# Kernel optimization log

Hardware: AMD Instinct MI355X
Metric: run time of the kernel (lower is better)

## Reference

```python
import jax, jax.numpy as jnp
import numpy as np

B, S, D = 2, 2048, 4096
H, KVH, HD = 32, 8, 128   # attention heads, kv heads, head_dim
GROUPS = H // KVH          # 4
SCALING = 0.08838834764831845  # attention_multiplier = 1/sqrt(head_dim)
NEG = -1e9


def _rope_tables(seq_len, head_dim, base=10000.0):
    half = head_dim // 2
    inv_freq = 1.0 / (base ** (np.arange(0, half, dtype=np.float32) / half))
    t = np.arange(seq_len, dtype=np.float32)
    freqs = np.outer(t, inv_freq)               # [S, half]
    emb = np.concatenate([freqs, freqs], axis=-1)  # [S, head_dim]
    return jnp.asarray(np.cos(emb)), jnp.asarray(np.sin(emb))


def setup_inputs() -> dict:
    key = jax.random.key(0)
    ks = jax.random.split(key, 6)
    hidden_states = jax.random.normal(ks[0], (B, S, D), dtype=jnp.float32)
    std = 0.02
    Wq = jax.random.normal(ks[1], (D, H * HD), dtype=jnp.float32) * std
    Wk = jax.random.normal(ks[2], (D, KVH * HD), dtype=jnp.float32) * std
    Wv = jax.random.normal(ks[3], (D, KVH * HD), dtype=jnp.float32) * std
    Wo = jax.random.normal(ks[4], (H * HD, D), dtype=jnp.float32) * std
    cos1, sin1 = _rope_tables(S, HD)
    cos = jnp.broadcast_to(cos1[None], (B, S, HD))
    sin = jnp.broadcast_to(sin1[None], (B, S, HD))
    # additive causal mask [B, 1, S, S]
    causal = jnp.where(jnp.tril(jnp.ones((S, S), dtype=bool)), 0.0, NEG).astype(jnp.float32)
    attention_mask = jnp.broadcast_to(causal[None, None], (B, 1, S, S))
    return {"hidden_states": hidden_states, "cos": cos, "sin": sin,
            "attention_mask": attention_mask, "Wq": Wq, "Wk": Wk, "Wv": Wv, "Wo": Wo}


def _rotate_half(x):
    x1, x2 = jnp.split(x, 2, axis=-1)
    return jnp.concatenate([-x2, x1], axis=-1)


def reference(hidden_states, cos, sin, attention_mask, Wq, Wk, Wv, Wo):
    b, s, _ = hidden_states.shape
    # projections (no bias), split into heads: [B, H, S, HD]
    q = jnp.einsum('bsd,de->bse', hidden_states, Wq).reshape(b, s, H, HD).transpose(0, 2, 1, 3)
    k = jnp.einsum('bsd,de->bse', hidden_states, Wk).reshape(b, s, KVH, HD).transpose(0, 2, 1, 3)
    v = jnp.einsum('bsd,de->bse', hidden_states, Wv).reshape(b, s, KVH, HD).transpose(0, 2, 1, 3)
    # RoPE (cos/sin unsqueezed on head dim)
    c = cos[:, None, :, :]
    sn = sin[:, None, :, :]
    q = q * c + _rotate_half(q) * sn
    k = k * c + _rotate_half(k) * sn
    # repeat_kv: [B, KVH, S, HD] -> [B, H, S, HD]
    k = jnp.repeat(k, GROUPS, axis=1)
    v = jnp.repeat(v, GROUPS, axis=1)
    # eager attention: full score matrix, additive mask, fp32 softmax
    scores = jnp.einsum('bhqd,bhkd->bhqk', q, k) * SCALING + attention_mask
    attn_weights = jax.nn.softmax(scores.astype(jnp.float32), axis=-1).astype(q.dtype)
    attn_output = jnp.einsum('bhqk,bhkd->bhqd', attn_weights, v)
    attn_output = attn_output.transpose(0, 2, 1, 3).reshape(b, s, H * HD)
    attn_output = jnp.einsum('bse,ed->bsd', attn_output, Wo)
    return attn_output, attn_weights
```

## Files before the change

### kernel.cpp

```cpp
#include <hip/hip_runtime.h>

typedef unsigned short u16;
typedef unsigned int u32;
typedef __attribute__((ext_vector_type(8))) short bf16x8;
typedef __attribute__((ext_vector_type(4))) float f32x4;

#define SCALING 0.08838834764831845f

__device__ __forceinline__ float bf2f(u16 u) {
  union { u32 i; float f; } v; v.i = ((u32)u) << 16; return v.f;
}
__device__ __forceinline__ u16 f2bf(float f) {
  union { float f; u32 i; } v; v.f = f;
  u32 x = v.i;
  return (u16)((x + 0x7fffu + ((x >> 16) & 1u)) >> 16);
}

__device__ __forceinline__ void gll16(const void* g, void* l) {
  __builtin_amdgcn_global_load_lds((const __attribute__((address_space(1))) void*)g,
                                   (__attribute__((address_space(3))) void*)l, 16, 0, 0);
}

__global__ void cast_f32_to_bf16(const float* __restrict__ in, u16* __restrict__ out, int n4) {
  int i = blockIdx.x * 256 + threadIdx.x;
  if (i >= n4) return;
  float4 v = ((const float4*)in)[i];
  ushort4 o;
  o.x = f2bf(v.x); o.y = f2bf(v.y); o.z = f2bf(v.z); o.w = f2bf(v.w);
  ((ushort4*)out)[i] = o;
}

__global__ void transpose_cast(const float* __restrict__ W, u16* __restrict__ WT, int Kd, int Nd) {
  __shared__ float tile[32][33];
  int n0 = blockIdx.x * 32, k0 = blockIdx.y * 32;
  int t = threadIdx.x;
  int r = t >> 3;
  int c = (t & 7) * 4;
  float4 v = *(const float4*)(W + (size_t)(k0 + r) * Nd + n0 + c);
  tile[r][c + 0] = v.x; tile[r][c + 1] = v.y; tile[r][c + 2] = v.z; tile[r][c + 3] = v.w;
  __syncthreads();
  ushort4 o;
  o.x = f2bf(tile[c + 0][r]); o.y = f2bf(tile[c + 1][r]);
  o.z = f2bf(tile[c + 2][r]); o.w = f2bf(tile[c + 3][r]);
  *(ushort4*)(WT + (size_t)(n0 + r) * Kd + k0 + c) = o;
}

template <bool OUT_F32>
__global__ __launch_bounds__(256) void gemm_bt(const u16* __restrict__ A, const u16* __restrict__ B,
                                               void* __restrict__ C, int M, int N, int K) {
  __shared__ __align__(16) u16 As[128 * 32];
  __shared__ __align__(16) u16 Bs[128 * 32];
  const int tid = threadIdx.x;
  const int lane = tid & 63;
  const int w = tid >> 6;
  const int wr = w >> 1, wc = w & 1;
  const int q = lane >> 4, cl = lane & 15;
  const int m0 = blockIdx.y * 128, n0 = blockIdx.x * 128;

  const int srow = w * 16 + (lane >> 2);
  const int schk = (lane & 3) * 8;
  const u16* Ag0 = A + (size_t)(m0 + srow) * K + schk;
  const u16* Ag1 = Ag0 + (size_t)64 * K;
  const u16* Bg0 = B + (size_t)(n0 + srow) * K + schk;
  const u16* Bg1 = Bg0 + (size_t)64 * K;
  u16* Asp = As + srow * 32 + schk;
  u16* Bsp = Bs + srow * 32 + schk;

  f32x4 zero4 = {0.f, 0.f, 0.f, 0.f};
  f32x4 acc[4][4];
#pragma unroll
  for (int mi = 0; mi < 4; ++mi)
#pragma unroll
    for (int ni = 0; ni < 4; ++ni) acc[mi][ni] = zero4;

  for (int kk = 0; kk < K; kk += 32) {
    gll16(Ag0 + kk, Asp);
    gll16(Ag1 + kk, Asp + 64 * 32);
    gll16(Bg0 + kk, Bsp);
    gll16(Bg1 + kk, Bsp + 64 * 32);
    __syncthreads();
    bf16x8 af[4], bfv[4];
#pragma unroll
    for (int mi = 0; mi < 4; ++mi)
      af[mi] = *(const bf16x8*)(As + (wr * 64 + mi * 16 + cl) * 32 + q * 8);
#pragma unroll
    for (int ni = 0; ni < 4; ++ni)
      bfv[ni] = *(const bf16x8*)(Bs + (wc * 64 + ni * 16 + cl) * 32 + q * 8);
#pragma unroll
    for (int mi = 0; mi < 4; ++mi)
#pragma unroll
      for (int ni = 0; ni < 4; ++ni)
        acc[mi][ni] = __builtin_amdgcn_mfma_f32_16x16x32_bf16(af[mi], bfv[ni], acc[mi][ni], 0, 0, 0);
    __syncthreads();
  }

#pragma unroll
  for (int mi = 0; mi < 4; ++mi)
#pragma unroll
    for (int ni = 0; ni < 4; ++ni) {
      int row = m0 + wr * 64 + mi * 16 + q * 4;
      int col = n0 + wc * 64 + ni * 16 + cl;
#pragma unroll
      for (int r = 0; r < 4; ++r) {
        if (OUT_F32)
          ((float*)C)[(size_t)(row + r) * N + col] = acc[mi][ni][r];
        else
          ((u16*)C)[(size_t)(row + r) * N + col] = f2bf(acc[mi][ni][r]);
      }
    }
}

__global__ void rope_kernel(u16* __restrict__ X, const float* __restrict__ cosb,
                            const float* __restrict__ sinb, int rowstride) {
  int row = blockIdx.x;
  int v = blockIdx.y * 256 + threadIdx.x;
  int d = v & 63, hh = v >> 6;
  size_t base = (size_t)row * rowstride + hh * 128 + d;
  float x1 = bf2f(X[base]);
  float x2 = bf2f(X[base + 64]);
  const float* cp = cosb + (size_t)row * 128;
  const float* sp = sinb + (size_t)row * 128;
  X[base]      = f2bf(x1 * cp[d]      - x2 * sp[d]);
  X[base + 64] = f2bf(x2 * cp[d + 64] + x1 * sp[d + 64]);
}

__global__ __launch_bounds__(512, 4) void attn_kernel(
    const u16* __restrict__ Qb, const u16* __restrict__ Kb, const u16* __restrict__ Vb,
    float* __restrict__ Wout, u16* __restrict__ AO) {
  const int qt = blockIdx.x;
  const int h = blockIdx.y;
  const int b = blockIdx.z;
  const int kvh = h >> 2;

  __shared__ __align__(16) u16 Ksm[2][64 * 128];
  __shared__ __align__(16) u32 Vt[128 * 32];
  __shared__ __align__(16) u16 Ps[128 * 64];
  __shared__ float l_lds[128];

  const int tid = threadIdx.x;
  const int lane = tid & 63;
  const int w = tid >> 6;
  const int wr = w >> 1, wc = w & 1;
  const int q = lane >> 4, cl = lane & 15;
  const int cx = cl & 7;

  const size_t qrow0 = (size_t)b * 2048 + qt * 128;
  const u16* Qh = Qb + qrow0 * 4096 + h * 128;
  const u16* Kh = Kb + ((size_t)b * 2048) * 1024 + kvh * 128;
  const u16* Vh = Vb + ((size_t)b * 2048) * 1024 + kvh * 128;

  bf16x8 qa[2][4];
#pragma unroll
  for (int mi = 0; mi < 2; ++mi) {
    const u16* qp = Qh + (size_t)(wr * 32 + mi * 16 + cl) * 4096 + q * 8;
#pragma unroll
    for (int kd = 0; kd < 4; ++kd) qa[mi][kd] = *(const bf16x8*)(qp + kd * 32);
  }

  if (tid < 128) l_lds[tid] = 0.f;

  const int srow = tid >> 4;
  const int kchunk = (tid & 15) ^ (srow & 7);
  const int njt = 2 * qt + 2;

  auto stageK = [&](int jt, int buf) {
    const u16* s0 = Kh + ((size_t)(jt * 64 + srow)) * 1024 + kchunk * 8;
    u16* d0 = Ksm[buf] + tid * 8;
    gll16(s0, d0);
    gll16(s0 + 32 * 1024, d0 + 4096);
  };

  f32x4 zero4 = {0.f, 0.f, 0.f, 0.f};

  float lpart[2][4];
#pragma unroll
  for (int mi = 0; mi < 2; ++mi)
#pragma unroll
    for (int r = 0; r < 4; ++r) lpart[mi][r] = 0.f;

  stageK(0, 0);
  for (int t = 0; t < njt; ++t) {
    __syncthreads();
    if (t + 1 < njt) stageK(t + 1, (t + 1) & 1);
    const u16* Kc = Ksm[t & 1];
    f32x4 acc[2][2];
#pragma unroll
    for (int mi = 0; mi < 2; ++mi)
#pragma unroll
      for (int ni = 0; ni < 2; ++ni) acc[mi][ni] = zero4;
    __builtin_amdgcn_s_setprio(1);
#pragma unroll
    for (int kd = 0; kd < 4; ++kd) {
      bf16x8 bk[2];
#pragma unroll
      for (int ni = 0; ni < 2; ++ni) {
        int row = wc * 32 + ni * 16 + cl;
        bk[ni] = *(const bf16x8*)(Kc + row * 128 + (((kd * 4 + q) ^ cx) << 3));
      }
#pragma unroll
      for (int mi = 0; mi < 2; ++mi)
#pragma unroll
        for (int ni = 0; ni < 2; ++ni)
          acc[mi][ni] = __builtin_amdgcn_mfma_f32_16x16x32_bf16(qa[mi][kd], bk[ni], acc[mi][ni], 0, 0, 0);
    }
    __builtin_amdgcn_s_setprio(0);
    if (t >= 2 * qt) {
#pragma unroll
      for (int mi = 0; mi < 2; ++mi)
#pragma unroll
        for (int r = 0; r < 4; ++r) {
          int ig = qt * 128 + wr * 32 + mi * 16 + q * 4 + r;
          float s = 0.f;
#pragma unroll
          for (int ni = 0; ni < 2; ++ni) {
            int jg = t * 64 + wc * 32 + ni * 16 + cl;
            s += (jg <= ig) ? __expf(acc[mi][ni][r] * SCALING) : 0.f;
          }
          lpart[mi][r] += s;
        }
    } else {
#pragma unroll
      for (int mi = 0; mi < 2; ++mi)
#pragma unroll
        for (int r = 0; r < 4; ++r) {
          float s = 0.f;
#pragma unroll
          for (int ni = 0; ni < 2; ++ni) s += __expf(acc[mi][ni][r] * SCALING);
          lpart[mi][r] += s;
        }
    }
  }
#pragma unroll
  for (int mi = 0; mi < 2; ++mi)
#pragma unroll
    for (int r = 0; r < 4; ++r) {
      float v = lpart[mi][r];
      v += __shfl_xor(v, 1, 64);
      v += __shfl_xor(v, 2, 64);
      v += __shfl_xor(v, 4, 64);
      v += __shfl_xor(v, 8, 64);
      if (cl == 0) atomicAdd(&l_lds[wr * 32 + mi * 16 + q * 4 + r], v);
    }
  __syncthreads();
  float rv[2][4];
#pragma unroll
  for (int mi = 0; mi < 2; ++mi)
#pragma unroll
    for (int r = 0; r < 4; ++r) rv[mi][r] = 1.f / l_lds[wr * 32 + mi * 16 + q * 4 + r];

  f32x4 oacc[2][4];
#pragma unroll
  for (int mi = 0; mi < 2; ++mi)
#pragma unroll
    for (int nd = 0; nd < 4; ++nd) oacc[mi][nd] = zero4;

  const int vp = tid >> 4;
  const int vc = tid & 15;
  const int vd0 = vc * 8;

  stageK(0, 0);
  for (int t = 0; t < njt; ++t) {
    __syncthreads();

    const u16* vsrc = Vh + ((size_t)(t * 64 + 2 * vp)) * 1024 + vd0;
    uint4 va = *(const uint4*)vsrc;
    uint4 vb4 = *(const uint4*)(vsrc + 1024);

    const u16* Kc = Ksm[t & 1];
    f32x4 acc[2][2];
#pragma unroll
    for (int mi = 0; mi < 2; ++mi)
#pragma unroll
      for (int ni = 0; ni < 2; ++ni) acc[mi][ni] = zero4;
    __builtin_amdgcn_s_setprio(1);
#pragma unroll
    for (int kd = 0; kd < 4; ++kd) {
      bf16x8 bk[2];
#pragma unroll
      for (int ni = 0; ni < 2; ++ni) {
        int row = wc * 32 + ni * 16 + cl;
        bk[ni] = *(const bf16x8*)(Kc + row * 128 + (((kd * 4 + q) ^ cx) << 3));
      }
#pragma unroll
      for (int mi = 0; mi < 2; ++mi)
#pragma unroll
        for (int ni = 0; ni < 2; ++ni)
          acc[mi][ni] = __builtin_amdgcn_mfma_f32_16x16x32_bf16(qa[mi][kd], bk[ni], acc[mi][ni], 0, 0, 0);
    }
    __builtin_amdgcn_s_setprio(0);

    {
      const u16* ah = (const u16*)&va;
      const u16* bh = (const u16*)&vb4;
#pragma unroll
      for (int kk = 0; kk < 8; ++kk) {
        int k = (kk + vc) & 7;
        int d = vd0 + k;
        Vt[d * 32 + ((((vp >> 2) ^ k) << 2) | (vp & 3))] = (u32)ah[k] | ((u32)bh[k] << 16);
      }
    }

    {
      bool diag = (t >= 2 * qt);
#pragma unroll
      for (int mi = 0; mi < 2; ++mi)
#pragma unroll
        for (int r = 0; r < 4; ++r) {
          int row = wr * 32 + mi * 16 + q * 4 + r;
          int ig = qt * 128 + row;
          float rvv = rv[mi][r];
#pragma unroll
          for (int ni = 0; ni < 2; ++ni) {
            int col = wc * 32 + ni * 16 + cl;
            float p = __expf(acc[mi][ni][r] * SCALING) * rvv;
            if (diag) { int jg = t * 64 + col; p = (jg <= ig) ? p : 0.f; }
            Ps[row * 64 + (((col >> 3) ^ (row & 7)) << 3) + (col & 7)] = f2bf(p);
          }
        }
    }

    if (t + 1 < njt) stageK(t + 1, (t + 1) & 1);

    asm volatile("s_waitcnt lgkmcnt(0)\n\ts_barrier" ::: "memory");

    {
      float* wb = Wout + (((size_t)(b * 32 + h) * 2048 + qt * 128) * 2048) + (size_t)t * 64;
#pragma unroll
      for (int it = 0; it < 2; ++it) {
        int cf = tid + it * 512;
        int row = cf >> 3;
        int ch = (cf & 7) * 8;
        bf16x8 pv8 = *(const bf16x8*)(Ps + row * 64 + (((ch >> 3) ^ (row & 7)) << 3));
        float4 o0 = {bf2f((u16)pv8[0]), bf2f((u16)pv8[1]), bf2f((u16)pv8[2]), bf2f((u16)pv8[3])};
        float4 o1 = {bf2f((u16)pv8[4]), bf2f((u16)pv8[5]), bf2f((u16)pv8[6]), bf2f((u16)pv8[7])};
        float* dp = wb + (size_t)row * 2048 + ch;
        *(float4*)dp = o0;
        *(float4*)(dp + 4) = o1;
      }
    }

    {
      __builtin_amdgcn_s_setprio(1);
#pragma unroll
      for (int ks = 0; ks < 2; ++ks) {
        bf16x8 pa[2], vbf[4];
#pragma unroll
        for (int mi = 0; mi < 2; ++mi) {
          int row = wr * 32 + mi * 16 + cl;
          pa[mi] = *(const bf16x8*)(Ps + row * 64 + (((ks * 4 + q) ^ cx) << 3));
        }
#pragma unroll
        for (int nd = 0; nd < 4; ++nd) {
          int d = wc * 64 + nd * 16 + cl;
          vbf[nd] = *(const bf16x8*)((const u16*)Vt + d * 64 + (((ks * 4 + q) ^ cx) << 3));
        }
#pragma unroll
        for (int mi = 0; mi < 2; ++mi)
#pragma unroll
          for (int nd = 0; nd < 4; ++nd)
            oacc[mi][nd] = __builtin_amdgcn_mfma_f32_16x16x32_bf16(pa[mi], vbf[nd], oacc[mi][nd], 0, 0, 0);
      }
      __builtin_amdgcn_s_setprio(0);
    }
  }

  {
    float* wb0 = Wout + (((size_t)(b * 32 + h) * 2048 + qt * 128) * 2048);
    float4 z = {0.f, 0.f, 0.f, 0.f};
    for (int jt = njt; jt < 32; ++jt) {
      float* wbz = wb0 + (size_t)jt * 64;
#pragma unroll
      for (int it = 0; it < 2; ++it) {
        int cf = tid + it * 512;
        int row = cf >> 3;
        int ch = (cf & 7) * 8;
        float* dp = wbz + (size_t)row * 2048 + ch;
        *(float4*)dp = z;
        *(float4*)(dp + 4) = z;
      }
    }
  }

#pragma unroll
  for (int mi = 0; mi < 2; ++mi)
#pragma unroll
    for (int nd = 0; nd < 4; ++nd) {
      int il = wr * 32 + mi * 16 + q * 4;
      int d = wc * 64 + nd * 16 + cl;
#pragma unroll
      for (int r = 0; r < 4; ++r)
        AO[(qrow0 + il + r) * 4096 + h * 128 + d] = f2bf(oacc[mi][nd][r]);
    }
}

extern "C" void kernel_launch(void* const* d_in, const int* in_sizes, int n_in,
                              void* d_out, int out_size, void* d_ws, size_t ws_size,
                              hipStream_t stream) {
  const float* hidden = (const float*)d_in[0];
  const float* cosb = (const float*)d_in[1];
  const float* sinb = (const float*)d_in[2];
  const float* Wq = (const float*)d_in[4];
  const float* Wk = (const float*)d_in[5];
  const float* Wv = (const float*)d_in[6];
  const float* Wo = (const float*)d_in[7];

  char* ws = (char*)d_ws;
  u16* hb  = (u16*)(ws);
  u16* WqT = (u16*)(ws + 33554432L);
  u16* WkT = (u16*)(ws + 67108864L);
  u16* WvT = (u16*)(ws + 75497472L);
  u16* WoT = (u16*)(ws + 83886080L);
  u16* Qb  = (u16*)(ws + 117440512L);
  u16* Kb  = (u16*)(ws + 150994944L);
  u16* Vb  = (u16*)(ws + 159383552L);
  u16* AO  = WqT;

  float* out0 = (float*)d_out;
  float* out1 = out0 + 16777216L;

  cast_f32_to_bf16<<<16384, 256, 0, stream>>>(hidden, hb, 4194304);
  transpose_cast<<<dim3(128, 128), 256, 0, stream>>>(Wq, WqT, 4096, 4096);
  transpose_cast<<<dim3(32, 128), 256, 0, stream>>>(Wk, WkT, 4096, 1024);
  transpose_cast<<<dim3(32, 128), 256, 0, stream>>>(Wv, WvT, 4096, 1024);
  transpose_cast<<<dim3(128, 128), 256, 0, stream>>>(Wo, WoT, 4096, 4096);

  gemm_bt<false><<<dim3(32, 32), 256, 0, stream>>>(hb, WqT, Qb, 4096, 4096, 4096);
  gemm_bt<false><<<dim3(8, 32), 256, 0, stream>>>(hb, WkT, Kb, 4096, 1024, 4096);
  gemm_bt<false><<<dim3(8, 32), 256, 0, stream>>>(hb, WvT, Vb, 4096, 1024, 4096);

  rope_kernel<<<dim3(4096, 8), 256, 0, stream>>>(Qb, cosb, sinb, 4096);
  rope_kernel<<<dim3(4096, 2), 256, 0, stream>>>(Kb, cosb, sinb, 1024);

  attn_kernel<<<dim3(16, 32, 2), 512, 0, stream>>>(Qb, Kb, Vb, out1, AO);

  gemm_bt<true><<<dim3(32, 32), 256, 0, stream>>>(AO, WoT, out0, 4096, 4096, 4096);
}
```

Baseline: 2.805 ms.

## Pair causal query tiles per block, map KV groups to XCDs, prefetch V

Each attention block now processes two query tiles (qp and 15-qp) so every block does the same causal work. A flat 512-block grid is remapped so that blocks sharing a (batch, kv-head) group land on the same XCD, which should improve L2 reuse of K/V. V rows for the next tile are now prefetched into registers during the current tile, with explicit waitcnt barriers. This halves the block count and adds register pressure, and it depends on the waitcnt counts being exactly right.

```diff
diff --git a/kernel.cpp b/kernel.cpp
--- a/kernel.cpp
+++ b/kernel.cpp
@@ -127,10 +127,13 @@
 __global__ __launch_bounds__(512, 4) void attn_kernel(
     const u16* __restrict__ Qb, const u16* __restrict__ Kb, const u16* __restrict__ Vb,
     float* __restrict__ Wout, u16* __restrict__ AO) {
-  const int qt = blockIdx.x;
-  const int h = blockIdx.y;
-  const int b = blockIdx.z;
-  const int kvh = h >> 2;
+  const int flat = blockIdx.x;
+  const int xcd = flat & 7, slot = flat >> 3;
+  const int grp = xcd * 2 + (slot >> 5);
+  const int mem = slot & 31;
+  const int b = grp & 1, kvh = grp >> 1;
+  const int h = kvh * 4 + (mem & 3);
+  const int qp = mem >> 2;
 
   __shared__ __align__(16) u16 Ksm[2][64 * 128];
   __shared__ __align__(16) u32 Vt[128 * 32];
@@ -144,24 +147,14 @@
   const int q = lane >> 4, cl = lane & 15;
   const int cx = cl & 7;
 
-  const size_t qrow0 = (size_t)b * 2048 + qt * 128;
-  const u16* Qh = Qb + qrow0 * 4096 + h * 128;
   const u16* Kh = Kb + ((size_t)b * 2048) * 1024 + kvh * 128;
   const u16* Vh = Vb + ((size_t)b * 2048) * 1024 + kvh * 128;
 
-  bf16x8 qa[2][4];
-#pragma unroll
-  for (int mi = 0; mi < 2; ++mi) {
-    const u16* qp = Qh + (size_t)(wr * 32 + mi * 16 + cl) * 4096 + q * 8;
-#pragma unroll
-    for (int kd = 0; kd < 4; ++kd) qa[mi][kd] = *(const bf16x8*)(qp + kd * 32);
-  }
-
-  if (tid < 128) l_lds[tid] = 0.f;
-
   const int srow = tid >> 4;
   const int kchunk = (tid & 15) ^ (srow & 7);
-  const int njt = 2 * qt + 2;
+  const int vp = tid >> 4;
+  const int vc = tid & 15;
+  const int vd0 = vc * 8;
 
   auto stageK = [&](int jt, int buf) {
     const u16* s0 = Kh + ((size_t)(jt * 64 + srow)) * 1024 + kchunk * 8;
@@ -172,225 +165,252 @@
 
   f32x4 zero4 = {0.f, 0.f, 0.f, 0.f};
 
-  float lpart[2][4];
-#pragma unroll
-  for (int mi = 0; mi < 2; ++mi)
-#pragma unroll
-    for (int r = 0; r < 4; ++r) lpart[mi][r] = 0.f;
-
-  stageK(0, 0);
-  for (int t = 0; t < njt; ++t) {
+  for (int half = 0; half < 2; ++half) {
+    const int qt = half ? (15 - qp) : qp;
+    const int njt = 2 * qt + 2;
+    const size_t qrow0 = (size_t)b * 2048 + qt * 128;
+    const u16* Qh = Qb + qrow0 * 4096 + h * 128;
+
     __syncthreads();
-    if (t + 1 < njt) stageK(t + 1, (t + 1) & 1);
-    const u16* Kc = Ksm[t & 1];
-    f32x4 acc[2][2];
+    if (tid < 128) l_lds[tid] = 0.f;
+
+    bf16x8 qa[2][4];
+#pragma unroll
+    for (int mi = 0; mi < 2; ++mi) {
+      const u16* qp_ = Qh + (size_t)(wr * 32 + mi * 16 + cl) * 4096 + q * 8;
+#pragma unroll
+      for (int kd = 0; kd < 4; ++kd) qa[mi][kd] = *(const bf16x8*)(qp_ + kd * 32);
+    }
+
+    float lpart[2][4];
 #pragma unroll
     for (int mi = 0; mi < 2; ++mi)
 #pragma unroll
-      for (int ni = 0; ni < 2; ++ni) acc[mi][ni] = zero4;
-    __builtin_amdgcn_s_setprio(1);
-#pragma unroll
-    for (int kd = 0; kd < 4; ++kd) {
-      bf16x8 bk[2];
-#pragma unroll
-      for (int ni = 0; ni < 2; ++ni) {
-        int row = wc * 32 + ni * 16 + cl;
-        bk[ni] = *(const bf16x8*)(Kc + row * 128 + (((kd * 4 + q) ^ cx) << 3));
-      }
+      for (int r = 0; r < 4; ++r) lpart[mi][r] = 0.f;
+
+    stageK(0, 0);
+    __syncthreads();
+    for (int t = 0; t < njt; ++t) {
+      if (t + 1 < njt) stageK(t + 1, (t + 1) & 1);
+      const u16* Kc = Ksm[t & 1];
+      f32x4 acc[2][2];
 #pragma unroll
       for (int mi = 0; mi < 2; ++mi)
 #pragma unroll
-        for (int ni = 0; ni < 2; ++ni)
-          acc[mi][ni] = __builtin_amdgcn_mfma_f32_16x16x32_bf16(qa[mi][kd], bk[ni], acc[mi][ni], 0, 0, 0);
-    }
-    __builtin_amdgcn_s_setprio(0);
-    if (t >= 2 * qt) {
+        for (int ni = 0; ni < 2; ++ni) acc[mi][ni] = zero4;
+      __builtin_amdgcn_s_setprio(1);
+#pragma unroll
+      for (int kd = 0; kd < 4; ++kd) {
+        bf16x8 bk[2];
+#pragma unroll
+        for (int ni = 0; ni < 2; ++ni) {
+          int row = wc * 32 + ni * 16 + cl;
+          bk[ni] = *(const bf16x8*)(Kc + row * 128 + (((kd * 4 + q) ^ cx) << 3));
+        }
+#pragma unroll
+        for (int mi = 0; mi < 2; ++mi)
+#pragma unroll
+          for (int ni = 0; ni < 2; ++ni)
+            acc[mi][ni] = __builtin_amdgcn_mfma_f32_16x16x32_bf16(qa[mi][kd], bk[ni], acc[mi][ni], 0, 0, 0);
+      }
+      __builtin_amdgcn_s_setprio(0);
+      if (t >= 2 * qt) {
+#pragma unroll
+        for (int mi = 0; mi < 2; ++mi)
+#pragma unroll
+          for (int r = 0; r < 4; ++r) {
+            int ig = qt * 128 + wr * 32 + mi * 16 + q * 4 + r;
+            float s = 0.f;
+#pragma unroll
+            for (int ni = 0; ni < 2; ++ni) {
+              int jg = t * 64 + wc * 32 + ni * 16 + cl;
+              s += (jg <= ig) ? __expf(acc[mi][ni][r] * SCALING) : 0.f;
+            }
+            lpart[mi][r] += s;
+          }
+      } else {
+#pragma unroll
+        for (int mi = 0; mi < 2; ++mi)
+#pragma unroll
+          for (int r = 0; r < 4; ++r) {
+            float s = 0.f;
+#pragma unroll
+            for (int ni = 0; ni < 2; ++ni) s += __expf(acc[mi][ni][r] * SCALING);
+            lpart[mi][r] += s;
+          }
+      }
+      if (t + 1 < njt) __syncthreads();
+    }
+#pragma unroll
+    for (int mi = 0; mi < 2; ++mi)
+#pragma unroll
+      for (int r = 0; r < 4; ++r) {
+        float v = lpart[mi][r];
+        v += __shfl_xor(v, 1, 64);
+        v += __shfl_xor(v, 2, 64);
+        v += __shfl_xor(v, 4, 64);
+        v += __shfl_xor(v, 8, 64);
+        if (cl == 0) atomicAdd(&l_lds[wr * 32 + mi * 16 + q * 4 + r], v);
+      }
+    __syncthreads();
+    float rv[2][4];
+#pragma unroll
+    for (int mi = 0; mi < 2; ++mi)
+#pragma unroll
+      for (int r = 0; r < 4; ++r) rv[mi][r] = 1.f / l_lds[wr * 32 + mi * 16 + q * 4 + r];
+
+    f32x4 oacc[2][4];
+#pragma unroll
+    for (int mi = 0; mi < 2; ++mi)
+#pragma unroll
+      for (int nd = 0; nd < 4; ++nd) oacc[mi][nd] = zero4;
+
+    uint4 vca, vcb, vna, vnb;
+    stageK(0, 0);
+    {
+      const u16* vsrc = Vh + ((size_t)(2 * vp)) * 1024 + vd0;
+      vca = *(const uint4*)vsrc;
+      vcb = *(const uint4*)(vsrc + 1024);
+    }
+    asm volatile("s_waitcnt vmcnt(2) lgkmcnt(0)\n\ts_barrier" ::: "memory");
+
+    for (int t = 0; t < njt; ++t) {
+      if (t + 1 < njt) {
+        stageK(t + 1, (t + 1) & 1);
+        const u16* vsrc = Vh + ((size_t)((t + 1) * 64 + 2 * vp)) * 1024 + vd0;
+        vna = *(const uint4*)vsrc;
+        vnb = *(const uint4*)(vsrc + 1024);
+      }
+
+      const u16* Kc = Ksm[t & 1];
+      f32x4 acc[2][2];
 #pragma unroll
       for (int mi = 0; mi < 2; ++mi)
 #pragma unroll
-        for (int r = 0; r < 4; ++r) {
-          int ig = qt * 128 + wr * 32 + mi * 16 + q * 4 + r;
-          float s = 0.f;
-#pragma unroll
-          for (int ni = 0; ni < 2; ++ni) {
-            int jg = t * 64 + wc * 32 + ni * 16 + cl;
-            s += (jg <= ig) ? __expf(acc[mi][ni][r] * SCALING) : 0.f;
+        for (int ni = 0; ni < 2; ++ni) acc[mi][ni] = zero4;
+      __builtin_amdgcn_s_setprio(1);
+#pragma unroll
+      for (int kd = 0; kd < 4; ++kd) {
+        bf16x8 bk[2];
+#pragma unroll
+        for (int ni = 0; ni < 2; ++ni) {
+          int row = wc * 32 + ni * 16 + cl;
+          bk[ni] = *(const bf16x8*)(Kc + row * 128 + (((kd * 4 + q) ^ cx) << 3));
+        }
+#pragma unroll
+        for (int mi = 0; mi < 2; ++mi)
+#pragma unroll
+          for (int ni = 0; ni < 2; ++ni)
+            acc[mi][ni] = __builtin_amdgcn_mfma_f32_16x16x32_bf16(qa[mi][kd], bk[ni], acc[mi][ni], 0, 0, 0);
+      }
+      __builtin_amdgcn_s_setprio(0);
+
+      {
+        const u16* ah = (const u16*)&vca;
+        const u16* bh = (const u16*)&vcb;
+#pragma unroll
+        for (int kk = 0; kk < 8; ++kk) {
+          int k = (kk + vc) & 7;
+          int d = vd0 + k;
+          Vt[d * 32 + ((((vp >> 2) ^ k) << 2) | (vp & 3))] = (u32)ah[k] | ((u32)bh[k] << 16);
+        }
+      }
+
+      {
+        bool diag = (t >= 2 * qt);
+#pragma unroll
+        for (int mi = 0; mi < 2; ++mi)
+#pragma unroll
+          for (int r = 0; r < 4; ++r) {
+            int row = wr * 32 + mi * 16 + q * 4 + r;
+            int ig = qt * 128 + row;
+            float rvv = rv[mi][r];
+#pragma unroll
+            for (int ni = 0; ni < 2; ++ni) {
+              int col = wc * 32 + ni * 16 + cl;
+              float p = __expf(acc[mi][ni][r] * SCALING) * rvv;
+              if (diag) { int jg = t * 64 + col; p = (jg <= ig) ? p : 0.f; }
+              Ps[row * 64 + (((col >> 3) ^ (row & 7)) << 3) + (col & 7)] = f2bf(p);
+            }
           }
-          lpart[mi][r] += s;
-        }
-    } else {
-#pragma unroll
-      for (int mi = 0; mi < 2; ++mi)
-#pragma unroll
-        for (int r = 0; r < 4; ++r) {
-          float s = 0.f;
-#pragma unroll
-          for (int ni = 0; ni < 2; ++ni) s += __expf(acc[mi][ni][r] * SCALING);
-          lpart[mi][r] += s;
-        }
-    }
+      }
+
+      asm volatile("s_waitcnt lgkmcnt(0)\n\ts_barrier" ::: "memory");
+
+      {
+        float* wb = Wout + (((size_t)(b * 32 + h) * 2048 + qt * 128) * 2048) + (size_t)t * 64;
+#pragma unroll
+        for (int it = 0; it < 2; ++it) {
+          int cf = tid + it * 512;
+          int row = cf >> 3;
+          int ch = (cf & 7) * 8;
+          bf16x8 pv8 = *(const bf16x8*)(Ps + row * 64 + (((ch >> 3) ^ (row & 7)) << 3));
+          float4 o0 = {bf2f((u16)pv8[0]), bf2f((u16)pv8[1]), bf2f((u16)pv8[2]), bf2f((u16)pv8[3])};
+          float4 o1 = {bf2f((u16)pv8[4]), bf2f((u16)pv8[5]), bf2f((u16)pv8[6]), bf2f((u16)pv8[7])};
+          float* dp = wb + (size_t)row * 2048 + ch;
+          *(float4*)dp = o0;
+          *(float4*)(dp + 4) = o1;
+        }
+      }
+
+      {
+        __builtin_amdgcn_s_setprio(1);
+#pragma unroll
+        for (int ks = 0; ks < 2; ++ks) {
+          bf16x8 pa[2], vbf[4];
+#pragma unroll
+          for (int mi = 0; mi < 2; ++mi) {
+            int row = wr * 32 + mi * 16 + cl;
+            pa[mi] = *(const bf16x8*)(Ps + row * 64 + (((ks * 4 + q) ^ cx) << 3));
+          }
+#pragma unroll
+          for (int nd = 0; nd < 4; ++nd) {
+            int d = wc * 64 + nd * 16 + cl;
+            vbf[nd] = *(const bf16x8*)((const u16*)Vt + d * 64 + (((ks * 4 + q) ^ cx) << 3));
+          }
+#pragma unroll
+          for (int mi = 0; mi < 2; ++mi)
+#pragma unroll
+            for (int nd = 0; nd < 4; ++nd)
+              oacc[mi][nd] = __builtin_amdgcn_mfma_f32_16x16x32_bf16(pa[mi], vbf[nd], oacc[mi][nd], 0, 0, 0);
+        }
+        __builtin_amdgcn_s_setprio(0);
+      }
+
+      if (t + 1 < njt) {
+        vca = vna; vcb = vnb;
+        asm volatile("s_waitcnt vmcnt(6) lgkmcnt(0)\n\ts_barrier" ::: "memory");
+      }
+    }
+
+    {
+      float* wb0 = Wout + (((size_t)(b * 32 + h) * 2048 + qt * 128) * 2048);
+      float4 z = {0.f, 0.f, 0.f, 0.f};
+      for (int jt = njt; jt < 32; ++jt) {
+        float* wbz = wb0 + (size_t)jt * 64;
+#pragma unroll
+        for (int it = 0; it < 2; ++it) {
+          int cf = tid + it * 512;
+          int row = cf >> 3;
+          int ch = (cf & 7) * 8;
+          float* dp = wbz + (size_t)row * 2048 + ch;
+          *(float4*)dp = z;
+          *(float4*)(dp + 4) = z;
+        }
+      }
+    }
+
+#pragma unroll
+    for (int mi = 0; mi < 2; ++mi)
+#pragma unroll
+      for (int nd = 0; nd < 4; ++nd) {
+        int il = wr * 32 + mi * 16 + q * 4;
+        int d = wc * 64 + nd * 16 + cl;
+#pragma unroll
+        for (int r = 0; r < 4; ++r)
+          AO[(qrow0 + il + r) * 4096 + h * 128 + d] = f2bf(oacc[mi][nd][r]);
+      }
   }
-#pragma unroll
-  for (int mi = 0; mi < 2; ++mi)
-#pragma unroll
-    for (int r = 0; r < 4; ++r) {
-      float v = lpart[mi][r];
-      v += __shfl_xor(v, 1, 64);
-      v += __shfl_xor(v, 2, 64);
-      v += __shfl_xor(v, 4, 64);
-      v += __shfl_xor(v, 8, 64);
-      if (cl == 0) atomicAdd(&l_lds[wr * 32 + mi * 16 + q * 4 + r], v);
-    }
-  __syncthreads();
-  float rv[2][4];
-#pragma unroll
-  for (int mi = 0; mi < 2; ++mi)
-#pragma unroll
-    for (int r = 0; r < 4; ++r) rv[mi][r] = 1.f / l_lds[wr * 32 + mi * 16 + q * 4 + r];
-
-  f32x4 oacc[2][4];
-#pragma unroll
-  for (int mi = 0; mi < 2; ++mi)
-#pragma unroll
-    for (int nd = 0; nd < 4; ++nd) oacc[mi][nd] = zero4;
-
-  const int vp = tid >> 4;
-  const int vc = tid & 15;
-  const int vd0 = vc * 8;
-
-  stageK(0, 0);
-  for (int t = 0; t < njt; ++t) {
-    __syncthreads();
-
-    const u16* vsrc = Vh + ((size_t)(t * 64 + 2 * vp)) * 1024 + vd0;
-    uint4 va = *(const uint4*)vsrc;
-    uint4 vb4 = *(const uint4*)(vsrc + 1024);
-
-    const u16* Kc = Ksm[t & 1];
-    f32x4 acc[2][2];
-#pragma unroll
-    for (int mi = 0; mi < 2; ++mi)
-#pragma unroll
-      for (int ni = 0; ni < 2; ++ni) acc[mi][ni] = zero4;
-    __builtin_amdgcn_s_setprio(1);
-#pragma unroll
-    for (int kd = 0; kd < 4; ++kd) {
-      bf16x8 bk[2];
-#pragma unroll
-      for (int ni = 0; ni < 2; ++ni) {
-        int row = wc * 32 + ni * 16 + cl;
-        bk[ni] = *(const bf16x8*)(Kc + row * 128 + (((kd * 4 + q) ^ cx) << 3));
-      }
-#pragma unroll
-      for (int mi = 0; mi < 2; ++mi)
-#pragma unroll
-        for (int ni = 0; ni < 2; ++ni)
-          acc[mi][ni] = __builtin_amdgcn_mfma_f32_16x16x32_bf16(qa[mi][kd], bk[ni], acc[mi][ni], 0, 0, 0);
-    }
-    __builtin_amdgcn_s_setprio(0);
-
-    {
-      const u16* ah = (const u16*)&va;
-      const u16* bh = (const u16*)&vb4;
-#pragma unroll
-      for (int kk = 0; kk < 8; ++kk) {
-        int k = (kk + vc) & 7;
-        int d = vd0 + k;
-        Vt[d * 32 + ((((vp >> 2) ^ k) << 2) | (vp & 3))] = (u32)ah[k] | ((u32)bh[k] << 16);
-      }
-    }
-
-    {
-      bool diag = (t >= 2 * qt);
-#pragma unroll
-      for (int mi = 0; mi < 2; ++mi)
-#pragma unroll
-        for (int r = 0; r < 4; ++r) {
-          int row = wr * 32 + mi * 16 + q * 4 + r;
-          int ig = qt * 128 + row;
-          float rvv = rv[mi][r];
-#pragma unroll
-          for (int ni = 0; ni < 2; ++ni) {
-            int col = wc * 32 + ni * 16 + cl;
-            float p = __expf(acc[mi][ni][r] * SCALING) * rvv;
-            if (diag) { int jg = t * 64 + col; p = (jg <= ig) ? p : 0.f; }
-            Ps[row * 64 + (((col >> 3) ^ (row & 7)) << 3) + (col & 7)] = f2bf(p);
-          }
-        }
-    }
-
-    if (t + 1 < njt) stageK(t + 1, (t + 1) & 1);
-
-    asm volatile("s_waitcnt lgkmcnt(0)\n\ts_barrier" ::: "memory");
-
-    {
-      float* wb = Wout + (((size_t)(b * 32 + h) * 2048 + qt * 128) * 2048) + (size_t)t * 64;
-#pragma unroll
-      for (int it = 0; it < 2; ++it) {
-        int cf = tid + it * 512;
-        int row = cf >> 3;
-        int ch = (cf & 7) * 8;
-        bf16x8 pv8 = *(const bf16x8*)(Ps + row * 64 + (((ch >> 3) ^ (row & 7)) << 3));
-        float4 o0 = {bf2f((u16)pv8[0]), bf2f((u16)pv8[1]), bf2f((u16)pv8[2]), bf2f((u16)pv8[3])};
-        float4 o1 = {bf2f((u16)pv8[4]), bf2f((u16)pv8[5]), bf2f((u16)pv8[6]), bf2f((u16)pv8[7])};
-        float* dp = wb + (size_t)row * 2048 + ch;
-        *(float4*)dp = o0;
-        *(float4*)(dp + 4) = o1;
-      }
-    }
-
-    {
-      __builtin_amdgcn_s_setprio(1);
-#pragma unroll
-      for (int ks = 0; ks < 2; ++ks) {
-        bf16x8 pa[2], vbf[4];
-#pragma unroll
-        for (int mi = 0; mi < 2; ++mi) {
-          int row = wr * 32 + mi * 16 + cl;
-          pa[mi] = *(const bf16x8*)(Ps + row * 64 + (((ks * 4 + q) ^ cx) << 3));
-        }
-#pragma unroll
-        for (int nd = 0; nd < 4; ++nd) {
-          int d = wc * 64 + nd * 16 + cl;
-          vbf[nd] = *(const bf16x8*)((const u16*)Vt + d * 64 + (((ks * 4 + q) ^ cx) << 3));
-        }
-#pragma unroll
-        for (int mi = 0; mi < 2; ++mi)
-#pragma unroll
-          for (int nd = 0; nd < 4; ++nd)
-            oacc[mi][nd] = __builtin_amdgcn_mfma_f32_16x16x32_bf16(pa[mi], vbf[nd], oacc[mi][nd], 0, 0, 0);
-      }
-      __builtin_amdgcn_s_setprio(0);
-    }
-  }
-
-  {
-    float* wb0 = Wout + (((size_t)(b * 32 + h) * 2048 + qt * 128) * 2048);
-    float4 z = {0.f, 0.f, 0.f, 0.f};
-    for (int jt = njt; jt < 32; ++jt) {
-      float* wbz = wb0 + (size_t)jt * 64;
-#pragma unroll
-      for (int it = 0; it < 2; ++it) {
-        int cf = tid + it * 512;
-        int row = cf >> 3;
-        int ch = (cf & 7) * 8;
-        float* dp = wbz + (size_t)row * 2048 + ch;
-        *(float4*)dp = z;
-        *(float4*)(dp + 4) = z;
-      }
-    }
-  }
-
-#pragma unroll
-  for (int mi = 0; mi < 2; ++mi)
-#pragma unroll
-    for (int nd = 0; nd < 4; ++nd) {
-      int il = wr * 32 + mi * 16 + q * 4;
-      int d = wc * 64 + nd * 16 + cl;
-#pragma unroll
-      for (int r = 0; r < 4; ++r)
-        AO[(qrow0 + il + r) * 4096 + h * 128 + d] = f2bf(oacc[mi][nd][r]);
-    }
 }
 
 extern "C" void kernel_launch(void* const* d_in, const int* in_sizes, int n_in,
@@ -431,7 +451,7 @@
   rope_kernel<<<dim3(4096, 8), 256, 0, stream>>>(Qb, cosb, sinb, 4096);
   rope_kernel<<<dim3(4096, 2), 256, 0, stream>>>(Kb, cosb, sinb, 1024);
 
-  attn_kernel<<<dim3(16, 32, 2), 512, 0, stream>>>(Qb, Kb, Vb, out1, AO);
+  attn_kernel<<<dim3(512), 512, 0, stream>>>(Qb, Kb, Vb, out1, AO);
 
   gemm_bt<true><<<dim3(32, 32), 256, 0, stream>>>(AO, WoT, out0, 4096, 4096, 4096);
 }
```

Result: faster. 2.509 ms (-10.5%).
